# Performance work log

Measured on AMD Instinct MI355X. Metric: run time of the kernel, lower is better.

The kernel has to match this reference:

```python
import jax, jax.numpy as jnp
import numpy as np

BETA = 0.25  # commitment_beta


def setup_inputs() -> dict:
    key = jax.random.key(0)
    k1, k2 = jax.random.split(key)
    B, C, H, W = 8, 256, 32, 32
    n_embed = 16384
    x = jax.random.normal(k1, (B, C, H, W), dtype=jnp.float32)
    # torch init: uniform_(-1/codebook_size, 1/codebook_size)
    weight = jax.random.uniform(k2, (n_embed, C), dtype=jnp.float32,
                                minval=-1.0 / n_embed, maxval=1.0 / n_embed)
    return {"x": x, "weight": weight}


def reference(x, weight):
    B, C, H, W = x.shape
    # b c h w -> b (h w) c
    xf = jnp.transpose(x, (0, 2, 3, 1)).reshape(B, H * W, C)
    flat = xf.reshape(-1, C)  # [N, C], N = B*H*W
    d = (jnp.sum(flat * flat, axis=1, keepdims=True)
         + jnp.sum(weight * weight, axis=1)[None, :]
         - 2.0 * flat @ weight.T)
    idx = jnp.argmin(d, axis=-1)          # [N]
    xq = weight[idx].reshape(B, H * W, C)  # codebook gather
    sg = jax.lax.stop_gradient
    loss = (BETA * jnp.mean((sg(xq) - xf) ** 2)
            + jnp.mean((xq - sg(xf)) ** 2))
    # straight-through estimator
    xq_st = xf + sg(xq - xf)
    # b (h w) c -> b c h w
    xq_img = jnp.transpose(xq_st.reshape(B, H, W, C), (0, 3, 1, 2))
    x_code = idx.reshape(B, H, W)
    return xq_img, loss, x_code
```

## Files before the change

### kernel.cpp

```cpp
#include <hip/hip_runtime.h>
#include <stdint.h>

#define NROW    8192
#define CDIM    256
#define NCODE   16384
#define MARGINF 1.6e-4f

typedef short short8 __attribute__((ext_vector_type(8)));
typedef float floatx4 __attribute__((ext_vector_type(4)));
typedef _Float16 half2v __attribute__((ext_vector_type(2)));

__device__ inline ushort f2bf(float f) {
    unsigned u = __builtin_bit_cast(unsigned, f);
    unsigned r = (u + 0x7fffu + ((u >> 16) & 1u)) >> 16;
    return (ushort)r;
}
__device__ inline unsigned fsort(float v) {
    unsigned u = __builtin_bit_cast(unsigned, v);
    return (u >> 31) ? ~u : (u | 0x80000000u);
}

__device__ inline void gl_lds16(const ushort* g, ushort* lds) {
    __builtin_amdgcn_global_load_lds(
        (const __attribute__((address_space(1))) unsigned int*)(g),
        (__attribute__((address_space(3))) unsigned int*)(lds),
        16, 0, 0);
}

__global__ __launch_bounds__(256) void prep_x(const float* __restrict__ x,
                                              float* __restrict__ xf32,
                                              ushort* __restrict__ xbf) {
    __shared__ float tile[32][33];
    const int b = blockIdx.x, ht = blockIdx.y, ct = blockIdx.z;
    const int t = threadIdx.x;
    const int hw0 = ht * 32, c0 = ct * 32;
    {
        const int cc = t >> 5, hh = t & 31;
        #pragma unroll
        for (int i = 0; i < 4; ++i) {
            int cl = cc + i * 8;
            tile[cl][hh] = x[((size_t)(b * 256 + c0 + cl) << 10) + hw0 + hh];
        }
    }
    __syncthreads();
    {
        const int col = t & 31, row = t >> 5;
        #pragma unroll
        for (int i = 0; i < 4; ++i) {
            int r = row + i * 8;
            float v = tile[col][r];
            size_t o = ((size_t)(b * 1024 + hw0 + r) << 8) + c0 + col;
            xf32[o] = v;
            xbf[o] = f2bf(v);
        }
    }
}

__global__ __launch_bounds__(256) void prep_w2(const float* __restrict__ w,
                                               ushort* __restrict__ wbf,
                                               float* __restrict__ S2a) {
#pragma clang fp contract(off)
    const int gt = blockIdx.x * 256 + threadIdx.x;
    const int j = gt >> 1, h = gt & 1;
    const float* a = w + ((size_t)j << 8) + h * 128;
    ushort* orow = wbf + ((size_t)j << 8) + h * 128;
    float r8[8];
    #pragma unroll
    for (int l = 0; l < 8; ++l) { float v = a[l]; r8[l] = v * v; }
    for (int i = 8; i < 128; i += 8) {
        #pragma unroll
        for (int l = 0; l < 8; ++l) { float v = a[i + l]; r8[l] = r8[l] + v * v; }
    }
    float hs = ((r8[0] + r8[1]) + (r8[2] + r8[3])) + ((r8[4] + r8[5]) + (r8[6] + r8[7]));
    float other = __shfl_xor(hs, 1);
    if (h == 0) S2a[j] = hs + other;
    for (int i = 0; i < 128; i += 8) {
        ushort u8[8];
        #pragma unroll
        for (int l = 0; l < 8; ++l) u8[l] = f2bf(a[i + l]);
        *(ushort4*)(orow + i)     = make_ushort4(u8[0], u8[1], u8[2], u8[3]);
        *(ushort4*)(orow + i + 4) = make_ushort4(u8[4], u8[5], u8[6], u8[7]);
    }
}

__global__ __launch_bounds__(256) void gemm_min(const ushort* __restrict__ Wb,
                                                const ushort* __restrict__ Xb,
                                                const float* __restrict__ S2a,
                                                ushort* __restrict__ bm16) {
    __shared__ __attribute__((aligned(16))) ushort As[8192];
    __shared__ __attribute__((aligned(16))) ushort Bs[8192];
    __shared__ __attribute__((aligned(16))) ushort stg[128 * 8];

    const int n0 = blockIdx.x * 128;
    const int j0 = blockIdx.y * 128;
    const int t  = threadIdx.x;
    const int wv = t >> 6, l = t & 63;
    const int wr = wv >> 1, wc = wv & 1;
    const int q  = l >> 4, c = l & 15;

    const int lr = l >> 3;
    const int lperm = (l & 7) ^ lr;
    const size_t gA0 = ((size_t)(j0 + wv * 32 + lr) << 8) + lperm * 8;
    const size_t gB0 = ((size_t)(n0 + wv * 32 + lr) << 8) + lperm * 8;
    const int ldsbase = wv * 2048;

    floatx4 acc[4][4];
    #pragma unroll
    for (int mi = 0; mi < 4; ++mi)
        #pragma unroll
        for (int ni = 0; ni < 4; ++ni)
            acc[mi][ni] = (floatx4){0.f, 0.f, 0.f, 0.f};

    for (int kb = 0; kb < 4; ++kb) {
        if (kb) __syncthreads();
        #pragma unroll
        for (int ca = 0; ca < 4; ++ca) {
            gl_lds16(Wb + gA0 + ca * 2048 + kb * 64, As + ldsbase + ca * 512);
            gl_lds16(Xb + gB0 + ca * 2048 + kb * 64, Bs + ldsbase + ca * 512);
        }
        __syncthreads();
        #pragma unroll
        for (int kk = 0; kk < 2; ++kk) {
            short8 af[4], bf[4];
            #pragma unroll
            for (int mi = 0; mi < 4; ++mi) {
                int row = wr * 64 + mi * 16 + c;
                int pos = (kk * 4 + q) ^ (c & 7);
                af[mi] = *(const short8*)&As[row * 64 + pos * 8];
            }
            #pragma unroll
            for (int ni = 0; ni < 4; ++ni) {
                int row = wc * 64 + ni * 16 + c;
                int pos = (kk * 4 + q) ^ (c & 7);
                bf[ni] = *(const short8*)&Bs[row * 64 + pos * 8];
            }
            #pragma unroll
            for (int mi = 0; mi < 4; ++mi)
                #pragma unroll
                for (int ni = 0; ni < 4; ++ni)
                    acc[mi][ni] = __builtin_amdgcn_mfma_f32_16x16x32_bf16(
                        af[mi], bf[ni], acc[mi][ni], 0, 0, 0);
        }
    }

    #pragma unroll
    for (int mi = 0; mi < 4; ++mi) {
        float4 s2 = *(const float4*)&S2a[j0 + wr * 64 + mi * 16 + (q << 2)];
        #pragma unroll
        for (int ni = 0; ni < 4; ++ni) {
            float m0 = fmaf(-2.f, acc[mi][ni][0], s2.x);
            float m1 = fmaf(-2.f, acc[mi][ni][1], s2.y);
            float m2 = fmaf(-2.f, acc[mi][ni][2], s2.z);
            float m3 = fmaf(-2.f, acc[mi][ni][3], s2.w);
            float m = fminf(fminf(m0, m1), fminf(m2, m3));
            m = fminf(m, __shfl_xor(m, 16));
            m = fminf(m, __shfl_xor(m, 32));
            if (q == 0) {
                int qr = wc * 64 + ni * 16 + c;
                stg[qr * 8 + wr * 4 + mi] =
                    __builtin_bit_cast(ushort, (_Float16)m);
            }
        }
    }
    __syncthreads();
    if (t < 128) {
        uint4 v = *(const uint4*)&stg[t * 8];
        *(uint4*)(bm16 + ((size_t)(n0 + t) << 10) + blockIdx.y * 8) = v;
    }
}

__global__ __launch_bounds__(256) void rescore2(const unsigned* __restrict__ bm32,
                                                const float* __restrict__ xf32,
                                                const float* __restrict__ w,
                                                const float* __restrict__ S2a,
                                                int* __restrict__ idxb,
                                                float* __restrict__ xcode,
                                                float* __restrict__ loss) {
#pragma clang fp contract(off)
    __shared__ float xrow[256];
    __shared__ float red[256];
    __shared__ unsigned long long redk[256];
    __shared__ short list[1024];
    __shared__ int np_;
    __shared__ float sS1[2];
    const int n = blockIdx.x, t = threadIdx.x;
    if (t == 0) np_ = 0;
    xrow[t] = xf32[((size_t)n << 8) + t];
    const uint2 bm = *(const uint2*)(bm32 + ((size_t)n << 9) + t * 2);
    const half2v ha = __builtin_bit_cast(half2v, bm.x);
    const half2v hb = __builtin_bit_cast(half2v, bm.y);
    float v4[4] = {(float)ha[0], (float)ha[1], (float)hb[0], (float)hb[1]};
    float m = fminf(fminf(v4[0], v4[1]), fminf(v4[2], v4[3]));
    red[t] = m;
    __syncthreads();
    for (int s = 128; s > 0; s >>= 1) {
        if (t < s) red[t] = fminf(red[t], red[t + s]);
        __syncthreads();
    }
    const float thr = red[0] + MARGINF;
    #pragma unroll
    for (int i = 0; i < 4; ++i)
        if (v4[i] <= thr) { int p = atomicAdd(&np_, 1); list[p] = (short)(t * 4 + i); }
    if (t < 2) {
        const float* a = &xrow[t * 128];
        float r8[8];
        #pragma unroll
        for (int l = 0; l < 8; ++l) { float v = a[l]; r8[l] = v * v; }
        for (int i = 8; i < 128; i += 8) {
            #pragma unroll
            for (int l = 0; l < 8; ++l) { float v = a[i + l]; r8[l] = r8[l] + v * v; }
        }
        sS1[t] = ((r8[0] + r8[1]) + (r8[2] + r8[3])) + ((r8[4] + r8[5]) + (r8[6] + r8[7]));
    }
    __syncthreads();
    const int total = np_ * 16;
    const float S1n = sS1[0] + sS1[1];
    unsigned long long best = ~0ull;
    for (int it = t; it < total; it += 256) {
        const int j = (int)list[it >> 4] * 16 + (it & 15);
        const float* wr_ = w + ((size_t)j << 8);
        float g = 0.f;
        for (int k = 0; k < 256; k += 4) {
            float4 wv = *(const float4*)(wr_ + k);
            g = fmaf(xrow[k],     wv.x, g);
            g = fmaf(xrow[k + 1], wv.y, g);
            g = fmaf(xrow[k + 2], wv.z, g);
            g = fmaf(xrow[k + 3], wv.w, g);
        }
        float d = (S1n + S2a[j]) - 2.0f * g;
        unsigned long long key = ((unsigned long long)fsort(d) << 32) | (unsigned)j;
        if (key < best) best = key;
    }
    redk[t] = best;
    __syncthreads();
    for (int s = 128; s > 0; s >>= 1) {
        if (t < s) { if (redk[t + s] < redk[t]) redk[t] = redk[t + s]; }
        __syncthreads();
    }
    const int J = (int)(redk[0] & 0xffffffffu);
    if (t == 0) {
        idxb[n] = J;
        xcode[n] = (float)J;
    }
    float dv = w[((size_t)J << 8) + t] - xrow[t];
    float lacc = dv * dv;
    #pragma unroll
    for (int off = 32; off; off >>= 1) lacc += __shfl_xor(lacc, off);
    if ((t & 63) == 0) red[t >> 6] = lacc;
    __syncthreads();
    if (t == 0) {
        float p = (red[0] + red[1]) + (red[2] + red[3]);
        atomicAdd(loss, p * (1.25f / 2097152.0f));
    }
}

__global__ __launch_bounds__(256) void outputs_k(const float* __restrict__ w,
                                                 const int* __restrict__ idxb,
                                                 float* __restrict__ out) {
    const int b = blockIdx.x, hq = blockIdx.y, cs = blockIdx.z;
    const int t = threadIdx.x;
    const int hw = hq * 256 + t;
    const int n = (b << 10) + hw;
    const int id = idxb[n];
    #pragma unroll 4
    for (int ci = 0; ci < 32; ++ci) {
        const int c_ = cs * 32 + ci;
        const size_t oo = ((size_t)((b << 8) + c_) << 10) + hw;
        out[oo] = w[((size_t)id << 8) + c_];
    }
}

extern "C" void kernel_launch(void* const* d_in, const int* in_sizes, int n_in,
                              void* d_out, int out_size, void* d_ws, size_t ws_size,
                              hipStream_t stream) {
    const float* x = (const float*)d_in[0];
    const float* w = (const float*)d_in[1];
    float* out = (float*)d_out;

    char* ws = (char*)d_ws;
    const size_t MB = 1024u * 1024u;
    ushort* xbf   = (ushort*)(ws);
    float*  xf32  = (float*) (ws + 4 * MB);
    ushort* wbf   = (ushort*)(ws + 12 * MB);
    float*  S2a   = (float*) (ws + 20 * MB);
    ushort* bm16  = (ushort*)(ws + 21 * MB);
    int*    idxb  = (int*)   (ws + 37 * MB);

    float* loss_ptr  = out + 2097152;
    float* xcode_ptr = out + 2097153;

    hipMemsetAsync((void*)loss_ptr, 0, 4, stream);

    prep_x  <<<dim3(8, 32, 8), 256, 0, stream>>>(x, xf32, xbf);
    prep_w2 <<<dim3(128),      256, 0, stream>>>(w, wbf, S2a);
    gemm_min<<<dim3(64, 128),  256, 0, stream>>>(wbf, xbf, S2a, bm16);
    rescore2<<<dim3(8192),     256, 0, stream>>>((const unsigned*)bm16, xf32, w,
                                                 S2a, idxb, xcode_ptr, loss_ptr);
    outputs_k<<<dim3(8, 4, 8), 256, 0, stream>>>(w, idxb, out);
}
```

Before: 299.4 us.

## Stage candidate codebook rows in LDS with coalesced loads and use wave-shuffle reductions

The rescore kernel now loads the candidate codebook rows cooperatively into a shared-memory tile, two 16-row blocks at a time with padding, using coalesced float4 loads. Previously each thread streamed its own 1 KB row from global memory. The tree reductions in LDS for the threshold and the argmin key are replaced by wave shuffles plus a 4-way combine, which removes many barriers. The cost is 33 KB of LDS per block, which may lower occupancy, and extra barriers per chunk of candidates. Only 32 threads compute dot products in each chunk.

Result: no change. 295.5 us (-1.3%).

```diff
diff --git a/kernel.cpp b/kernel.cpp
--- a/kernel.cpp
+++ b/kernel.cpp
@@ -169,7 +169,7 @@
     }
 }
 
-__global__ __launch_bounds__(256) void rescore2(const unsigned* __restrict__ bm32,
+__global__ __launch_bounds__(256) void rescore3(const ushort* __restrict__ bm16,
                                                 const float* __restrict__ xf32,
                                                 const float* __restrict__ w,
                                                 const float* __restrict__ S2a,
@@ -178,26 +178,29 @@
                                                 float* __restrict__ loss) {
 #pragma clang fp contract(off)
     __shared__ float xrow[256];
-    __shared__ float red[256];
-    __shared__ unsigned long long redk[256];
+    __shared__ float wpart[4];
+    __shared__ unsigned long long kpart[4];
     __shared__ short list[1024];
     __shared__ int np_;
     __shared__ float sS1[2];
+    __shared__ float wtile[2 * 16 * 260];
+
     const int n = blockIdx.x, t = threadIdx.x;
+    const int wv = t >> 6, l = t & 63;
     if (t == 0) np_ = 0;
     xrow[t] = xf32[((size_t)n << 8) + t];
-    const uint2 bm = *(const uint2*)(bm32 + ((size_t)n << 9) + t * 2);
-    const half2v ha = __builtin_bit_cast(half2v, bm.x);
-    const half2v hb = __builtin_bit_cast(half2v, bm.y);
-    float v4[4] = {(float)ha[0], (float)ha[1], (float)hb[0], (float)hb[1]};
+    const ushort4 bmv = *(const ushort4*)(bm16 + ((size_t)n << 10) + t * 4);
+    float v4[4] = {(float)__builtin_bit_cast(_Float16, bmv.x),
+                   (float)__builtin_bit_cast(_Float16, bmv.y),
+                   (float)__builtin_bit_cast(_Float16, bmv.z),
+                   (float)__builtin_bit_cast(_Float16, bmv.w)};
     float m = fminf(fminf(v4[0], v4[1]), fminf(v4[2], v4[3]));
-    red[t] = m;
-    __syncthreads();
-    for (int s = 128; s > 0; s >>= 1) {
-        if (t < s) red[t] = fminf(red[t], red[t + s]);
-        __syncthreads();
-    }
-    const float thr = red[0] + MARGINF;
+    #pragma unroll
+    for (int off = 1; off <= 32; off <<= 1) m = fminf(m, __shfl_xor(m, off));
+    if (l == 0) wpart[wv] = m;
+    __syncthreads();
+    const float thr = fminf(fminf(wpart[0], wpart[1]),
+                            fminf(wpart[2], wpart[3])) + MARGINF;
     #pragma unroll
     for (int i = 0; i < 4; ++i)
         if (v4[i] <= thr) { int p = atomicAdd(&np_, 1); list[p] = (short)(t * 4 + i); }
@@ -205,39 +208,56 @@
         const float* a = &xrow[t * 128];
         float r8[8];
         #pragma unroll
-        for (int l = 0; l < 8; ++l) { float v = a[l]; r8[l] = v * v; }
+        for (int lo = 0; lo < 8; ++lo) { float v = a[lo]; r8[lo] = v * v; }
         for (int i = 8; i < 128; i += 8) {
             #pragma unroll
-            for (int l = 0; l < 8; ++l) { float v = a[i + l]; r8[l] = r8[l] + v * v; }
+            for (int lo = 0; lo < 8; ++lo) { float v = a[i + lo]; r8[lo] = r8[lo] + v * v; }
         }
         sS1[t] = ((r8[0] + r8[1]) + (r8[2] + r8[3])) + ((r8[4] + r8[5]) + (r8[6] + r8[7]));
     }
     __syncthreads();
-    const int total = np_ * 16;
+
     const float S1n = sS1[0] + sS1[1];
+    const int nblk = np_;
     unsigned long long best = ~0ull;
-    for (int it = t; it < total; it += 256) {
-        const int j = (int)list[it >> 4] * 16 + (it & 15);
-        const float* wr_ = w + ((size_t)j << 8);
-        float g = 0.f;
-        for (int k = 0; k < 256; k += 4) {
-            float4 wv = *(const float4*)(wr_ + k);
-            g = fmaf(xrow[k],     wv.x, g);
-            g = fmaf(xrow[k + 1], wv.y, g);
-            g = fmaf(xrow[k + 2], wv.z, g);
-            g = fmaf(xrow[k + 3], wv.w, g);
-        }
-        float d = (S1n + S2a[j]) - 2.0f * g;
-        unsigned long long key = ((unsigned long long)fsort(d) << 32) | (unsigned)j;
-        if (key < best) best = key;
-    }
-    redk[t] = best;
-    __syncthreads();
-    for (int s = 128; s > 0; s >>= 1) {
-        if (t < s) { if (redk[t + s] < redk[t]) redk[t] = redk[t + s]; }
+    for (int c0 = 0; c0 < nblk; c0 += 2) {
+        const int nb = (nblk - c0) < 2 ? (nblk - c0) : 2;
+        for (int r = 0; r < nb * 4; ++r) {
+            int flat = r * 1024 + t * 4;
+            int row = flat >> 8;
+            int k = flat & 255;
+            int j = (int)list[c0 + (row >> 4)] * 16 + (row & 15);
+            *(float4*)&wtile[row * 260 + k] = *(const float4*)&w[((size_t)j << 8) + k];
+        }
         __syncthreads();
-    }
-    const int J = (int)(redk[0] & 0xffffffffu);
+        if (t < nb * 16) {
+            const int j = (int)list[c0 + (t >> 4)] * 16 + (t & 15);
+            const float* wr_ = &wtile[t * 260];
+            float g = 0.f;
+            for (int k = 0; k < 256; k += 4) {
+                float4 wvv = *(const float4*)(wr_ + k);
+                g = fmaf(xrow[k],     wvv.x, g);
+                g = fmaf(xrow[k + 1], wvv.y, g);
+                g = fmaf(xrow[k + 2], wvv.z, g);
+                g = fmaf(xrow[k + 3], wvv.w, g);
+            }
+            float d = (S1n + S2a[j]) - 2.0f * g;
+            unsigned long long key = ((unsigned long long)fsort(d) << 32) | (unsigned)j;
+            if (key < best) best = key;
+        }
+        __syncthreads();
+    }
+
+    #pragma unroll
+    for (int off = 1; off <= 32; off <<= 1) {
+        unsigned long long o = __shfl_xor(best, off);
+        if (o < best) best = o;
+    }
+    if (l == 0) kpart[wv] = best;
+    __syncthreads();
+    unsigned long long k01 = kpart[0] < kpart[1] ? kpart[0] : kpart[1];
+    unsigned long long k23 = kpart[2] < kpart[3] ? kpart[2] : kpart[3];
+    const int J = (int)((k01 < k23 ? k01 : k23) & 0xffffffffu);
     if (t == 0) {
         idxb[n] = J;
         xcode[n] = (float)J;
@@ -245,11 +265,11 @@
     float dv = w[((size_t)J << 8) + t] - xrow[t];
     float lacc = dv * dv;
     #pragma unroll
-    for (int off = 32; off; off >>= 1) lacc += __shfl_xor(lacc, off);
-    if ((t & 63) == 0) red[t >> 6] = lacc;
+    for (int off = 1; off <= 32; off <<= 1) lacc += __shfl_xor(lacc, off);
+    if (l == 0) wpart[wv] = lacc;
     __syncthreads();
     if (t == 0) {
-        float p = (red[0] + red[1]) + (red[2] + red[3]);
+        float p = (wpart[0] + wpart[1]) + (wpart[2] + wpart[3]);
         atomicAdd(loss, p * (1.25f / 2097152.0f));
     }
 }
@@ -294,7 +314,7 @@
     prep_x  <<<dim3(8, 32, 8), 256, 0, stream>>>(x, xf32, xbf);
     prep_w2 <<<dim3(128),      256, 0, stream>>>(w, wbf, S2a);
     gemm_min<<<dim3(64, 128),  256, 0, stream>>>(wbf, xbf, S2a, bm16);
-    rescore2<<<dim3(8192),     256, 0, stream>>>((const unsigned*)bm16, xf32, w,
-                                                 S2a, idxb, xcode_ptr, loss_ptr);
+    rescore3<<<dim3(8192),     256, 0, stream>>>(bm16, xf32, w, S2a, idxb,
+                                                 xcode_ptr, loss_ptr);
     outputs_k<<<dim3(8, 4, 8), 256, 0, stream>>>(w, idxb, out);
 }
```

## Rescore one row per wavefront with shuffle reductions instead of block barriers

Applied to the files above, without the earlier changes.

The rescore kernel now gives each 64-lane wavefront its own row, four rows per 256-thread block, in place of one row per block. All min and argmin reductions and the loss sum use wavefront shuffles rather than LDS trees with __syncthreads, and loss atomics now fire once per row. This removes many block barriers and cuts the number of launched blocks. The cost is less parallelism per row, since candidate dot products are spread over 64 lanes instead of 256. The candidate list is also capped at 128 tiles, which could drop true candidates when many ties fall near the threshold.

Measured after the change: 310.4 us. +3.7%, slower.

```diff
diff --git a/kernel.cpp b/kernel.cpp
--- a/kernel.cpp
+++ b/kernel.cpp
@@ -169,7 +169,7 @@
     }
 }
 
-__global__ __launch_bounds__(256) void rescore2(const unsigned* __restrict__ bm32,
+__global__ __launch_bounds__(256) void rescore4(const ushort* __restrict__ bm16,
                                                 const float* __restrict__ xf32,
                                                 const float* __restrict__ w,
                                                 const float* __restrict__ S2a,
@@ -177,81 +177,90 @@
                                                 float* __restrict__ xcode,
                                                 float* __restrict__ loss) {
 #pragma clang fp contract(off)
-    __shared__ float xrow[256];
-    __shared__ float red[256];
-    __shared__ unsigned long long redk[256];
-    __shared__ short list[1024];
-    __shared__ int np_;
-    __shared__ float sS1[2];
-    const int n = blockIdx.x, t = threadIdx.x;
-    if (t == 0) np_ = 0;
-    xrow[t] = xf32[((size_t)n << 8) + t];
-    const uint2 bm = *(const uint2*)(bm32 + ((size_t)n << 9) + t * 2);
-    const half2v ha = __builtin_bit_cast(half2v, bm.x);
-    const half2v hb = __builtin_bit_cast(half2v, bm.y);
-    float v4[4] = {(float)ha[0], (float)ha[1], (float)hb[0], (float)hb[1]};
-    float m = fminf(fminf(v4[0], v4[1]), fminf(v4[2], v4[3]));
-    red[t] = m;
-    __syncthreads();
-    for (int s = 128; s > 0; s >>= 1) {
-        if (t < s) red[t] = fminf(red[t], red[t + s]);
-        __syncthreads();
-    }
-    const float thr = red[0] + MARGINF;
-    #pragma unroll
-    for (int i = 0; i < 4; ++i)
-        if (v4[i] <= thr) { int p = atomicAdd(&np_, 1); list[p] = (short)(t * 4 + i); }
-    if (t < 2) {
-        const float* a = &xrow[t * 128];
-        float r8[8];
-        #pragma unroll
-        for (int l = 0; l < 8; ++l) { float v = a[l]; r8[l] = v * v; }
-        for (int i = 8; i < 128; i += 8) {
-            #pragma unroll
-            for (int l = 0; l < 8; ++l) { float v = a[i + l]; r8[l] = r8[l] + v * v; }
-        }
-        sS1[t] = ((r8[0] + r8[1]) + (r8[2] + r8[3])) + ((r8[4] + r8[5]) + (r8[6] + r8[7]));
-    }
-    __syncthreads();
-    const int total = np_ * 16;
-    const float S1n = sS1[0] + sS1[1];
+    __shared__ float xs[4][256];
+    __shared__ short list[4][128];
+    __shared__ int ncand[4];
+
+    const int t = threadIdx.x, wv = t >> 6, l = t & 63;
+    const int n = blockIdx.x * 4 + wv;
+    if (l == 0) ncand[wv] = 0;
+
+    const float4 xv = *(const float4*)&xf32[((size_t)n << 8) + l * 4];
+    *(float4*)&xs[wv][l * 4] = xv;
+
+    const uint4* bp = (const uint4*)(bm16 + ((size_t)n << 10) + l * 16);
+    const uint4 b0 = bp[0], b1 = bp[1];
+    float vals[16];
+    {
+        unsigned uu[8] = {b0.x, b0.y, b0.z, b0.w, b1.x, b1.y, b1.z, b1.w};
+        #pragma unroll
+        for (int i = 0; i < 8; ++i) {
+            half2v h = __builtin_bit_cast(half2v, uu[i]);
+            vals[2 * i]     = (float)h[0];
+            vals[2 * i + 1] = (float)h[1];
+        }
+    }
+    float vmin = vals[0];
+    #pragma unroll
+    for (int i = 1; i < 16; ++i) vmin = fminf(vmin, vals[i]);
+    #pragma unroll
+    for (int off = 1; off <= 32; off <<= 1) vmin = fminf(vmin, __shfl_xor(vmin, off));
+    const float thr = vmin + MARGINF;
+    #pragma unroll
+    for (int i = 0; i < 16; ++i)
+        if (vals[i] <= thr) {
+            int p = atomicAdd(&ncand[wv], 1);
+            if (p < 128) list[wv][p] = (short)(l * 16 + i);
+        }
+
+    float racc = 0.f;
+    if (l < 16) {
+        const float* a_ = &xs[wv][(l >> 3) * 128];
+        const int ai = l & 7;
+        float v = a_[ai];
+        racc = v * v;
+        for (int i = 8; i < 128; i += 8) { v = a_[i + ai]; racc = racc + v * v; }
+    }
+    racc = racc + __shfl_xor(racc, 1);
+    racc = racc + __shfl_xor(racc, 2);
+    racc = racc + __shfl_xor(racc, 4);
+    racc = racc + __shfl_xor(racc, 8);
+    const float S1n = __shfl(racc, 0);
+
+    const int ntot = (ncand[wv] < 128 ? ncand[wv] : 128) * 16;
     unsigned long long best = ~0ull;
-    for (int it = t; it < total; it += 256) {
-        const int j = (int)list[it >> 4] * 16 + (it & 15);
+    for (int s = l; s < ntot; s += 64) {
+        const int j = (int)list[wv][s >> 4] * 16 + (s & 15);
         const float* wr_ = w + ((size_t)j << 8);
         float g = 0.f;
+        #pragma unroll 8
         for (int k = 0; k < 256; k += 4) {
-            float4 wv = *(const float4*)(wr_ + k);
-            g = fmaf(xrow[k],     wv.x, g);
-            g = fmaf(xrow[k + 1], wv.y, g);
-            g = fmaf(xrow[k + 2], wv.z, g);
-            g = fmaf(xrow[k + 3], wv.w, g);
+            float4 wvv = *(const float4*)(wr_ + k);
+            g = fmaf(xs[wv][k],     wvv.x, g);
+            g = fmaf(xs[wv][k + 1], wvv.y, g);
+            g = fmaf(xs[wv][k + 2], wvv.z, g);
+            g = fmaf(xs[wv][k + 3], wvv.w, g);
         }
         float d = (S1n + S2a[j]) - 2.0f * g;
         unsigned long long key = ((unsigned long long)fsort(d) << 32) | (unsigned)j;
         if (key < best) best = key;
     }
-    redk[t] = best;
-    __syncthreads();
-    for (int s = 128; s > 0; s >>= 1) {
-        if (t < s) { if (redk[t + s] < redk[t]) redk[t] = redk[t + s]; }
-        __syncthreads();
-    }
-    const int J = (int)(redk[0] & 0xffffffffu);
-    if (t == 0) {
+    #pragma unroll
+    for (int off = 1; off <= 32; off <<= 1) {
+        unsigned long long o = __shfl_xor(best, off);
+        if (o < best) best = o;
+    }
+    const int J = (int)(best & 0xffffffffu);
+    if (l == 0) {
         idxb[n] = J;
         xcode[n] = (float)J;
     }
-    float dv = w[((size_t)J << 8) + t] - xrow[t];
-    float lacc = dv * dv;
-    #pragma unroll
-    for (int off = 32; off; off >>= 1) lacc += __shfl_xor(lacc, off);
-    if ((t & 63) == 0) red[t >> 6] = lacc;
-    __syncthreads();
-    if (t == 0) {
-        float p = (red[0] + red[1]) + (red[2] + red[3]);
-        atomicAdd(loss, p * (1.25f / 2097152.0f));
-    }
+    const float4 wj = *(const float4*)&w[((size_t)J << 8) + l * 4];
+    float d0 = wj.x - xv.x, d1 = wj.y - xv.y, d2 = wj.z - xv.z, d3 = wj.w - xv.w;
+    float lacc = (d0 * d0 + d1 * d1) + (d2 * d2 + d3 * d3);
+    #pragma unroll
+    for (int off = 1; off <= 32; off <<= 1) lacc += __shfl_xor(lacc, off);
+    if (l == 0) atomicAdd(loss, lacc * (1.25f / 2097152.0f));
 }
 
 __global__ __launch_bounds__(256) void outputs_k(const float* __restrict__ w,
@@ -294,7 +303,7 @@
     prep_x  <<<dim3(8, 32, 8), 256, 0, stream>>>(x, xf32, xbf);
     prep_w2 <<<dim3(128),      256, 0, stream>>>(w, wbf, S2a);
     gemm_min<<<dim3(64, 128),  256, 0, stream>>>(wbf, xbf, S2a, bm16);
-    rescore2<<<dim3(8192),     256, 0, stream>>>((const unsigned*)bm16, xf32, w,
-                                                 S2a, idxb, xcode_ptr, loss_ptr);
+    rescore4<<<dim3(2048),     256, 0, stream>>>(bm16, xf32, w, S2a, idxb,
+                                                 xcode_ptr, loss_ptr);
     outputs_k<<<dim3(8, 4, 8), 256, 0, stream>>>(w, idxb, out);
 }
```
